# Optimization experiments

Hardware: AMD Instinct MI355X
Metric: run time of the kernel (lower is better)

The kernel has to match this reference:

```python
import jax, jax.numpy as jnp
import numpy as np

H = 16        # num query heads
KV = 4        # num kv heads
D = 128       # head_dim


def setup_inputs() -> dict:
    key = jax.random.key(0)
    ks = jax.random.split(key, 5)
    B, S, E = 2, 2048, 2048
    kv_dim = KV * D
    s = 0.02
    return {
        "x": jax.random.normal(ks[0], (B, S, E), dtype=jnp.float32),
        "Wq": jax.random.normal(ks[1], (E, E), dtype=jnp.float32) * s,
        "Wk": jax.random.normal(ks[2], (kv_dim, E), dtype=jnp.float32) * s,
        "Wv": jax.random.normal(ks[3], (kv_dim, E), dtype=jnp.float32) * s,
        "Wo": jax.random.normal(ks[4], (E, E), dtype=jnp.float32) * s,
    }


def reference(x, Wq, Wk, Wv, Wo):
    B, S, E = x.shape
    rep = H // KV  # num_queries_per_kv
    # projections (torch Linear: y = x @ W.T), then [B, heads, S, D]
    q = (x @ Wq.T).reshape(B, S, H, D).transpose(0, 2, 1, 3)
    k = (x @ Wk.T).reshape(B, S, KV, D).transpose(0, 2, 1, 3)
    v = (x @ Wv.T).reshape(B, S, KV, D).transpose(0, 2, 1, 3)
    # GQA: repeat kv heads to match query heads (repeat_interleave on head dim)
    k = jnp.repeat(k, rep, axis=1)
    v = jnp.repeat(v, rep, axis=1)
    scores = jnp.einsum('bhsd,bhtd->bhst', q, k) / jnp.sqrt(jnp.float32(D))
    causal = jnp.tril(jnp.ones((S, S), dtype=bool))
    scores = jnp.where(causal, scores, jnp.finfo(x.dtype).min)
    w = jax.nn.softmax(scores, axis=-1)
    attn = jnp.einsum('bhst,bhtd->bhsd', w, v)  # [B,H,S,D]
    attn = attn.transpose(0, 2, 1, 3).reshape(B, S, E)
    return attn @ Wo.T
```

## Files before the change

kernel.cpp:

```cpp
#include <hip/hip_runtime.h>
#include <hip/hip_bf16.h>
#include <stdint.h>

typedef __attribute__((ext_vector_type(8))) short bf16x8;
typedef __attribute__((ext_vector_type(4))) float f32x4;

#define DEV static __device__ __forceinline__

DEV unsigned short f2bf(float f) {
  union { float f; uint32_t u; } a; a.f = f;
  uint32_t u = a.u;
  return (unsigned short)((u + 0x7FFFu + ((u >> 16) & 1u)) >> 16);
}

DEV void gll16(const void* g, void* l) {
  __builtin_amdgcn_global_load_lds((const __attribute__((address_space(1))) void*)g,
                                   (__attribute__((address_space(3))) void*)l,
                                   16, 0, 0);
}

__global__ __launch_bounds__(256) void cvt_kernel(const float* __restrict__ src,
                                                  unsigned short* __restrict__ dst,
                                                  int n4) {
  int i = blockIdx.x * 256 + threadIdx.x;
  if (i >= n4) return;
  float4 f = reinterpret_cast<const float4*>(src)[i];
  ushort4 o;
  o.x = f2bf(f.x); o.y = f2bf(f.y); o.z = f2bf(f.z); o.w = f2bf(f.w);
  reinterpret_cast<ushort4*>(dst)[i] = o;
}

DEV void storeC(float* p, float v) { *p = v; }
DEV void storeC(unsigned short* p, float v) { *p = f2bf(v); }

template <typename OutT>
__global__ __launch_bounds__(256) void gemm_bt(const unsigned short* __restrict__ A,
                                               const unsigned short* __restrict__ B,
                                               OutT* __restrict__ C,
                                               int M, int N, int K) {
  __shared__ unsigned short As[128 * 32];
  __shared__ unsigned short Bs[128 * 32];
  const int tid = threadIdx.x;
  const int lane = tid & 63;
  const int wave = tid >> 6;
  const int bm = blockIdx.x, bn = blockIdx.y;
  const int wr = wave >> 1, wc = wave & 1;
  const int lrow = lane >> 2, lch = lane & 3;
  const int fr = lane & 15, fg = lane >> 4;

  f32x4 acc[4][4];
#pragma unroll
  for (int m = 0; m < 4; ++m)
#pragma unroll
    for (int n = 0; n < 4; ++n) acc[m][n] = (f32x4){0.f, 0.f, 0.f, 0.f};

  const unsigned short* ga0 = A + (size_t)(bm * 128 + wave * 32 + lrow) * K + lch * 8;
  const unsigned short* gb0 = B + (size_t)(bn * 128 + wave * 32 + lrow) * K + lch * 8;
  char* la0 = (char*)As + wave * 32 * 64;
  char* lb0 = (char*)Bs + wave * 32 * 64;

  for (int k0 = 0; k0 < K; k0 += 32) {
    gll16(ga0 + k0, la0);
    gll16(ga0 + k0 + 16 * K, la0 + 16 * 64);
    gll16(gb0 + k0, lb0);
    gll16(gb0 + k0 + 16 * K, lb0 + 16 * 64);
    __syncthreads();
    bf16x8 af[4], bfr[4];
#pragma unroll
    for (int m = 0; m < 4; ++m)
      af[m] = *(const bf16x8*)((const char*)As + (wr * 64 + m * 16 + fr) * 64 + fg * 16);
#pragma unroll
    for (int n = 0; n < 4; ++n)
      bfr[n] = *(const bf16x8*)((const char*)Bs + (wc * 64 + n * 16 + fr) * 64 + fg * 16);
#pragma unroll
    for (int m = 0; m < 4; ++m)
#pragma unroll
      for (int n = 0; n < 4; ++n)
        acc[m][n] = __builtin_amdgcn_mfma_f32_16x16x32_bf16(af[m], bfr[n], acc[m][n], 0, 0, 0);
    __syncthreads();
  }

#pragma unroll
  for (int m = 0; m < 4; ++m)
#pragma unroll
    for (int n = 0; n < 4; ++n)
#pragma unroll
      for (int r = 0; r < 4; ++r) {
        const int row = bm * 128 + wr * 64 + m * 16 + fg * 4 + r;
        const int col = bn * 128 + wc * 64 + n * 16 + fr;
        storeC(&C[(size_t)row * N + col], acc[m][n][r]);
      }
}


DEV void attn_tile(const unsigned short* __restrict__ Ks,
                   const unsigned short* __restrict__ Vt,
                   const bf16x8 qf[4], f32x4 oacc[8],
                   float& m_run, float& l_run,
                   int kv0, int q0w, int c, int g) {
  const float SCALE = 0.08838834764831845f;
  const int qg = q0w + c;
  int nbp = (q0w + 16 - kv0) >> 4;
  nbp = nbp < 0 ? 0 : (nbp > 4 ? 4 : nbp);
  if (nbp <= 0) return;

  f32x4 p[4];
#pragma unroll
  for (int nb = 0; nb < 4; ++nb) p[nb] = (f32x4){0.f, 0.f, 0.f, 0.f};
  const bool dm = (kv0 + 63 > q0w);
#pragma unroll
  for (int nb = 0; nb < 4; ++nb)
    if (nb < nbp) {
      f32x4 s = (f32x4){0.f, 0.f, 0.f, 0.f};
#pragma unroll
      for (int kk = 0; kk < 4; ++kk) {
        const int row = nb * 16 + c;
        const int colB = (kk * 64 + g * 16) ^ ((row & 7) << 4);
        bf16x8 kf = *(const bf16x8*)((const char*)Ks + row * 256 + colB);
        s = __builtin_amdgcn_mfma_f32_16x16x32_bf16(kf, qf[kk], s, 0, 0, 0);
      }
#pragma unroll
      for (int r = 0; r < 4; ++r) {
        float sv = s[r] * SCALE;
        if (dm && (kv0 + nb * 16 + g * 4 + r > qg)) sv = -1e30f;
        p[nb][r] = sv;
      }
    }
  float rmax = -1e30f;
#pragma unroll
  for (int nb = 0; nb < 4; ++nb)
    if (nb < nbp)
#pragma unroll
      for (int r = 0; r < 4; ++r) rmax = fmaxf(rmax, p[nb][r]);
  rmax = fmaxf(rmax, __shfl_xor(rmax, 16));
  rmax = fmaxf(rmax, __shfl_xor(rmax, 32));
  const float mnew = fmaxf(m_run, rmax);
  const float alpha = __expf(m_run - mnew);
  float rs = 0.f;
#pragma unroll
  for (int nb = 0; nb < 4; ++nb)
    if (nb < nbp)
#pragma unroll
      for (int r = 0; r < 4; ++r) {
        const float e = __expf(p[nb][r] - mnew);
        p[nb][r] = e;
        rs += e;
      }
  rs += __shfl_xor(rs, 16);
  rs += __shfl_xor(rs, 32);
  l_run = l_run * alpha + rs;
  m_run = mnew;
#pragma unroll
  for (int nd = 0; nd < 8; ++nd) oacc[nd] *= alpha;
#pragma unroll
  for (int w = 0; w < 2; ++w)
    if (w * 2 < nbp) {
      union { bf16x8 v; unsigned short u[8]; } pf;
#pragma unroll
      for (int j = 0; j < 8; ++j) {
        const int kl = g * 8 + j;
        const int src = c + (((kl >> 2) & 3) << 4);
        const float a0 = __shfl(p[w * 2 + 0][j & 3], src);
        const float a1 = __shfl(p[w * 2 + 1][j & 3], src);
        pf.u[j] = f2bf((kl & 16) ? a1 : a0);
      }
#pragma unroll
      for (int nd = 0; nd < 8; ++nd) {
        bf16x8 vf = *(const bf16x8*)((const char*)Vt +
                      ((nd * 16 + c) * 72 + w * 32 + g * 8) * 2);
        oacc[nd] = __builtin_amdgcn_mfma_f32_16x16x32_bf16(vf, pf.v, oacc[nd], 0, 0, 0);
      }
    }
}

__global__ __launch_bounds__(256) void attn_kernel(const unsigned short* __restrict__ qkv,
                                                   unsigned short* __restrict__ ob) {
  const int S = 2048;
  const int QKVS = 3072;
  __shared__ unsigned short Ks[64 * 128];
  __shared__ unsigned short Vt[128 * 72];
  const int tid = threadIdx.x;
  const int lane = tid & 63;
  const int wave = tid >> 6;
  const int b = blockIdx.z, h = blockIdx.y;
  const int tiA = blockIdx.x, tiB = 31 - tiA;
  const int kvh = h >> 2;
  const int c = lane & 15, g = lane >> 4;
  const int q0Aw = tiA * 64 + wave * 16;
  const int q0Bw = tiB * 64 + wave * 16;

  bf16x8 qfA[4], qfB[4];
  {
    const unsigned short* qpA = qkv + (size_t)(b * S + q0Aw + c) * QKVS + h * 128 + g * 8;
    const unsigned short* qpB = qkv + (size_t)(b * S + q0Bw + c) * QKVS + h * 128 + g * 8;
#pragma unroll
    for (int kk = 0; kk < 4; ++kk) {
      qfA[kk] = *(const bf16x8*)(qpA + kk * 32);
      qfB[kk] = *(const bf16x8*)(qpB + kk * 32);
    }
  }
  f32x4 oaccA[8], oaccB[8];
#pragma unroll
  for (int nd = 0; nd < 8; ++nd) {
    oaccA[nd] = (f32x4){0.f, 0.f, 0.f, 0.f};
    oaccB[nd] = (f32x4){0.f, 0.f, 0.f, 0.f};
  }
  float mA = -1e30f, lA = 0.f, mB = -1e30f, lB = 0.f;

  const int ntile = tiB + 1;
  for (int t = 0; t < ntile; ++t) {
    const int kv0 = t * 64;
    __syncthreads();
#pragma unroll
    for (int i = 0; i < 4; ++i) {
      const int r0 = i * 16 + wave * 4;
      const int row = r0 + g;
      const int ch = c ^ (row & 7);
      const unsigned short* gk = qkv + (size_t)(b * S + kv0 + row) * QKVS + 2048 + kvh * 128 + ch * 8;
      gll16(gk, (char*)Ks + r0 * 256);
    }
#pragma unroll
    for (int ii = 0; ii < 4; ++ii) {
      const int d0 = wave * 32 + ii * 8;
      const unsigned short* gv = qkv + (size_t)(b * S + kv0 + lane) * QKVS + 2560 + kvh * 128 + d0;
      union { int4 i4; unsigned short u[8]; } vv;
      vv.i4 = *(const int4*)gv;
#pragma unroll
      for (int j = 0; j < 8; ++j) Vt[(d0 + j) * 72 + lane] = vv.u[j];
    }
    __syncthreads();
    if (t <= tiA) attn_tile(Ks, Vt, qfA, oaccA, mA, lA, kv0, q0Aw, c, g);
    attn_tile(Ks, Vt, qfB, oaccB, mB, lB, kv0, q0Bw, c, g);
  }

  {
    const float inv = 1.f / lA;
    unsigned short* op = ob + ((size_t)(b * S + q0Aw + c) * 16 + h) * 128;
#pragma unroll
    for (int nd = 0; nd < 8; ++nd)
#pragma unroll
      for (int r = 0; r < 4; ++r)
        op[nd * 16 + g * 4 + r] = f2bf(oaccA[nd][r] * inv);
  }
  {
    const float inv = 1.f / lB;
    unsigned short* op = ob + ((size_t)(b * S + q0Bw + c) * 16 + h) * 128;
#pragma unroll
    for (int nd = 0; nd < 8; ++nd)
#pragma unroll
      for (int r = 0; r < 4; ++r)
        op[nd * 16 + g * 4 + r] = f2bf(oaccB[nd][r] * inv);
  }
}

extern "C" void kernel_launch(void* const* d_in, const int* in_sizes, int n_in,
                              void* d_out, int out_size, void* d_ws, size_t ws_size,
                              hipStream_t stream) {
  (void)in_sizes; (void)n_in; (void)out_size; (void)ws_size;
  const float* x  = (const float*)d_in[0];
  const float* Wq = (const float*)d_in[1];
  const float* Wk = (const float*)d_in[2];
  const float* Wv = (const float*)d_in[3];
  const float* Wo = (const float*)d_in[4];
  float* out = (float*)d_out;

  const int B = 2, S = 2048, E = 2048;
  const int M = B * S;
  const int KVDIM = 512;
  const int NQKV = E + 2 * KVDIM;

  char* p = (char*)d_ws;
  unsigned short* xb   = (unsigned short*)p; p += (size_t)M * E * 2;
  unsigned short* wqb  = (unsigned short*)p; p += (size_t)E * E * 2;
  unsigned short* wkb  = (unsigned short*)p; p += (size_t)KVDIM * E * 2;
  unsigned short* wvb  = (unsigned short*)p; p += (size_t)KVDIM * E * 2;
  unsigned short* wob  = (unsigned short*)p; p += (size_t)E * E * 2;
  unsigned short* qkvbuf = (unsigned short*)p; p += (size_t)M * NQKV * 2;
  unsigned short* abuf   = (unsigned short*)p; p += (size_t)M * E * 2;

  {
    int n4;
    n4 = (M * E) / 4;     cvt_kernel<<<(n4 + 255) / 256, 256, 0, stream>>>(x,  xb,  n4);
    n4 = (E * E) / 4;     cvt_kernel<<<(n4 + 255) / 256, 256, 0, stream>>>(Wq, wqb, n4);
    n4 = (KVDIM * E) / 4; cvt_kernel<<<(n4 + 255) / 256, 256, 0, stream>>>(Wk, wkb, n4);
    n4 = (KVDIM * E) / 4; cvt_kernel<<<(n4 + 255) / 256, 256, 0, stream>>>(Wv, wvb, n4);
    n4 = (E * E) / 4;     cvt_kernel<<<(n4 + 255) / 256, 256, 0, stream>>>(Wo, wob, n4);
  }

  dim3 blk(256);
  gemm_bt<unsigned short><<<dim3(M / 128, NQKV / 128), blk, 0, stream>>>(xb, wqb, qkvbuf, M, NQKV, E);
  attn_kernel<<<dim3(16, 16, B), blk, 0, stream>>>(qkvbuf, abuf);
  gemm_bt<float><<<dim3(M / 128, E / 128), blk, 0, stream>>>(abuf, wob, out, M, E, E);
}
```

Measured before the change: 350.9 us.

## Use exp2 softmax with lazy rescaling and LDS-staged P in attention

Folds log2(e) into the score scale and uses the hardware v_exp_f32 (exp2) directly. The running max is only raised when it grows by more than 8, which skips most oacc rescales. The probability-fragment transpose moves from many lane shuffles with scalar bf16 conversions to packed bf16 conversion and a write/read through a per-wave LDS buffer. s_setprio is raised around the MFMA sections. The cost is extra LDS traffic and reliance on compiler barriers rather than explicit wave syncs for the P buffer, which is safe only because lanes within a wave execute in lockstep. Letting values exceed the running max by up to 2^8 carries some risk in fp32 and bf16 range.

```diff
diff --git a/kernel.cpp b/kernel.cpp
--- a/kernel.cpp
+++ b/kernel.cpp
@@ -11,6 +11,18 @@
   union { float f; uint32_t u; } a; a.f = f;
   uint32_t u = a.u;
   return (unsigned short)((u + 0x7FFFu + ((u >> 16) & 1u)) >> 16);
+}
+
+DEV float exp2_hw(float x) {
+  float r;
+  asm("v_exp_f32 %0, %1" : "=v"(r) : "v"(x));
+  return r;
+}
+
+DEV uint32_t pk_bf16(float lo, float hi) {
+  uint32_t r;
+  asm("v_cvt_pk_bf16_f32 %0, %1, %2" : "=v"(r) : "v"(lo), "v"(hi));
+  return r;
 }
 
 DEV void gll16(const void* g, void* l) {
@@ -95,10 +107,11 @@
 
 DEV void attn_tile(const unsigned short* __restrict__ Ks,
                    const unsigned short* __restrict__ Vt,
+                   unsigned short* __restrict__ Plw,
                    const bf16x8 qf[4], f32x4 oacc[8],
                    float& m_run, float& l_run,
                    int kv0, int q0w, int c, int g) {
-  const float SCALE = 0.08838834764831845f;
+  const float SCALE2 = 0.12754296f;
   const int qg = q0w + c;
   int nbp = (q0w + 16 - kv0) >> 4;
   nbp = nbp < 0 ? 0 : (nbp > 4 ? 4 : nbp);
@@ -108,6 +121,7 @@
 #pragma unroll
   for (int nb = 0; nb < 4; ++nb) p[nb] = (f32x4){0.f, 0.f, 0.f, 0.f};
   const bool dm = (kv0 + 63 > q0w);
+  __builtin_amdgcn_s_setprio(1);
 #pragma unroll
   for (int nb = 0; nb < 4; ++nb)
     if (nb < nbp) {
@@ -121,11 +135,12 @@
       }
 #pragma unroll
       for (int r = 0; r < 4; ++r) {
-        float sv = s[r] * SCALE;
+        float sv = s[r] * SCALE2;
         if (dm && (kv0 + nb * 16 + g * 4 + r > qg)) sv = -1e30f;
         p[nb][r] = sv;
       }
     }
+  __builtin_amdgcn_s_setprio(0);
   float rmax = -1e30f;
 #pragma unroll
   for (int nb = 0; nb < 4; ++nb)
@@ -134,43 +149,50 @@
       for (int r = 0; r < 4; ++r) rmax = fmaxf(rmax, p[nb][r]);
   rmax = fmaxf(rmax, __shfl_xor(rmax, 16));
   rmax = fmaxf(rmax, __shfl_xor(rmax, 32));
-  const float mnew = fmaxf(m_run, rmax);
-  const float alpha = __expf(m_run - mnew);
+  if (rmax > m_run + 8.f) {
+    const float al = exp2_hw(m_run - rmax);
+    m_run = rmax;
+    l_run *= al;
+#pragma unroll
+    for (int nd = 0; nd < 8; ++nd) oacc[nd] *= al;
+  }
   float rs = 0.f;
 #pragma unroll
   for (int nb = 0; nb < 4; ++nb)
-    if (nb < nbp)
-#pragma unroll
-      for (int r = 0; r < 4; ++r) {
-        const float e = __expf(p[nb][r] - mnew);
-        p[nb][r] = e;
+#pragma unroll
+    for (int r = 0; r < 4; ++r) {
+      float e = 0.f;
+      if (nb < nbp) {
+        e = exp2_hw(p[nb][r] - m_run);
         rs += e;
       }
+      p[nb][r] = e;
+    }
   rs += __shfl_xor(rs, 16);
   rs += __shfl_xor(rs, 32);
-  l_run = l_run * alpha + rs;
-  m_run = mnew;
-#pragma unroll
-  for (int nd = 0; nd < 8; ++nd) oacc[nd] *= alpha;
+  l_run += rs;
+  asm volatile("" ::: "memory");
+#pragma unroll
+  for (int nb = 0; nb < 4; ++nb) {
+    uint2 u;
+    u.x = pk_bf16(p[nb][0], p[nb][1]);
+    u.y = pk_bf16(p[nb][2], p[nb][3]);
+    *reinterpret_cast<uint2*>(Plw + c * 72 + nb * 16 + g * 4) = u;
+  }
+  asm volatile("" ::: "memory");
+  __builtin_amdgcn_s_setprio(1);
 #pragma unroll
   for (int w = 0; w < 2; ++w)
     if (w * 2 < nbp) {
-      union { bf16x8 v; unsigned short u[8]; } pf;
-#pragma unroll
-      for (int j = 0; j < 8; ++j) {
-        const int kl = g * 8 + j;
-        const int src = c + (((kl >> 2) & 3) << 4);
-        const float a0 = __shfl(p[w * 2 + 0][j & 3], src);
-        const float a1 = __shfl(p[w * 2 + 1][j & 3], src);
-        pf.u[j] = f2bf((kl & 16) ? a1 : a0);
-      }
+      bf16x8 pb = *(const bf16x8*)(Plw + c * 72 + w * 32 + g * 8);
 #pragma unroll
       for (int nd = 0; nd < 8; ++nd) {
         bf16x8 vf = *(const bf16x8*)((const char*)Vt +
                       ((nd * 16 + c) * 72 + w * 32 + g * 8) * 2);
-        oacc[nd] = __builtin_amdgcn_mfma_f32_16x16x32_bf16(vf, pf.v, oacc[nd], 0, 0, 0);
-      }
-    }
+        oacc[nd] = __builtin_amdgcn_mfma_f32_16x16x32_bf16(vf, pb, oacc[nd], 0, 0, 0);
+      }
+    }
+  __builtin_amdgcn_s_setprio(0);
 }
 
 __global__ __launch_bounds__(256) void attn_kernel(const unsigned short* __restrict__ qkv,
@@ -179,6 +201,7 @@
   const int QKVS = 3072;
   __shared__ unsigned short Ks[64 * 128];
   __shared__ unsigned short Vt[128 * 72];
+  __shared__ unsigned short Pl[4 * 16 * 72];
   const int tid = threadIdx.x;
   const int lane = tid & 63;
   const int wave = tid >> 6;
@@ -188,6 +211,7 @@
   const int c = lane & 15, g = lane >> 4;
   const int q0Aw = tiA * 64 + wave * 16;
   const int q0Bw = tiB * 64 + wave * 16;
+  unsigned short* Plw = Pl + wave * 16 * 72;
 
   bf16x8 qfA[4], qfB[4];
   {
@@ -229,8 +253,8 @@
       for (int j = 0; j < 8; ++j) Vt[(d0 + j) * 72 + lane] = vv.u[j];
     }
     __syncthreads();
-    if (t <= tiA) attn_tile(Ks, Vt, qfA, oaccA, mA, lA, kv0, q0Aw, c, g);
-    attn_tile(Ks, Vt, qfB, oaccB, mB, lB, kv0, q0Bw, c, g);
+    if (t <= tiA) attn_tile(Ks, Vt, Plw, qfA, oaccA, mA, lA, kv0, q0Aw, c, g);
+    attn_tile(Ks, Vt, Plw, qfB, oaccB, mB, lB, kv0, q0Bw, c, g);
   }
 
   {
```

Result: faster. 336.8 us (-4.0%).
